# Performance work log

Hardware: AMD Instinct MI355X
Metric: run time of the kernel (lower is better)

## Reference

```python
import jax, jax.numpy as jnp
import numpy as np

TAU = 1.0
ATOL = 1e-06
MAX_ITER = 64  # bisection halves the bracket each iter; 64 iters reaches fp32 precision
N_WORKERS = 64
D = 2097152  # 2**21 coordinates


def setup_inputs() -> dict:
    key = jax.random.key(0)
    y = jax.random.normal(key, (N_WORKERS, D), dtype=jnp.float32)
    return {"y": y}


def reference(y) -> jnp.ndarray:
    # Coordinate-wise smooth (erf-based) median via bisection.
    # torch code transposes y and reduces over the last dim; equivalently we
    # reduce over the worker axis (axis 0) and keep per-coordinate state [d].
    xl = jnp.min(y, axis=0)  # [d] lower bracket
    xg = jnp.max(y, axis=0)  # [d] upper bracket

    def body(_, carry):
        xl, xg = carry
        xm = 0.5 * (xl + xg)                                  # [d]
        fm = jnp.sum(jax.lax.erf((y - xm) / TAU), axis=0)     # [d]
        left = fm > 0
        xl = jnp.where(left, xm, xl)
        xg = jnp.where(left, xg, xm)
        return xl, xg

    # Fixed trip count (no host-sync early exit). After MAX_ITER=64 halvings the
    # bracket width is far below the torch atol=1e-6 break threshold, so the
    # result matches the torch early-exit version to well within atol.
    xl, xg = jax.lax.fori_loop(0, MAX_ITER, body, (xl, xg))
    return 0.5 * (xl + xg)  # [d]
```

## Files before the change

### kernel.cpp

```cpp
#include <hip/hip_runtime.h>

typedef float v2f __attribute__((ext_vector_type(2)));

#define NW 64
#define NP 32
#define MAX_EVALS 8
#define FREEZE_TOL 7e-3f

__global__ __launch_bounds__(256, 4) void damed_median_kernel(
    const float* __restrict__ y, float* __restrict__ out, int D) {
  int d = blockIdx.x * blockDim.x + threadIdx.x;
  if (d >= D) return;

  v2f v[NP];
  v2f vmin = {3.4e38f, 3.4e38f}, vmax = {-3.4e38f, -3.4e38f}, sum2 = {0.f, 0.f};
#pragma unroll
  for (int p = 0; p < NP; ++p) {
    v2f t;
    t.x = y[(size_t)(2 * p) * (size_t)D + (size_t)d];
    t.y = y[(size_t)(2 * p + 1) * (size_t)D + (size_t)d];
    v[p] = t;
    vmin = __builtin_elementwise_min(vmin, t);
    vmax = __builtin_elementwise_max(vmax, t);
    sum2 += t;
  }
  float xl = fminf(vmin.x, vmin.y);
  float xg = fmaxf(vmax.x, vmax.y);
  float x = (sum2.x + sum2.y) * (1.0f / NW);
  x = fminf(fmaxf(x, xl), xg);

  const float B1 = 0.278393f, B2 = 0.230389f, B3 = 0.000972f, B4 = 0.078108f;
  const v2f one2 = {1.f, 1.f};
  const v2f Q1 = {B1, B1}, Q2 = {B2, B2}, Q3 = {B3, B3}, Q4 = {B4, B4};
  const v2f P1 = {B1, B1}, P2 = {2 * B2, 2 * B2};
  const v2f P3 = {3 * B3, 3 * B3}, P4 = {4 * B4, 4 * B4};

  auto evalF = [&](float xc) -> float {
    v2f fmA = {0.f, 0.f}, fmB = {0.f, 0.f};
    v2f nx = {-xc, -xc};
#pragma unroll
    for (int p = 0; p < NP; p += 2) {
      v2f tA = v[p] + nx;
      v2f tB = v[p + 1] + nx;
      v2f aA = __builtin_elementwise_max(tA, -tA);
      v2f aB = __builtin_elementwise_max(tB, -tB);
      v2f qA = __builtin_elementwise_fma(aA, Q4, Q3);
      v2f qB = __builtin_elementwise_fma(aB, Q4, Q3);
      qA = __builtin_elementwise_fma(aA, qA, Q2);
      qB = __builtin_elementwise_fma(aB, qB, Q2);
      qA = __builtin_elementwise_fma(aA, qA, Q1);
      qB = __builtin_elementwise_fma(aB, qB, Q1);
      qA = __builtin_elementwise_fma(aA, qA, one2);
      qB = __builtin_elementwise_fma(aB, qB, one2);
      v2f rA, rB;
      rA.x = __builtin_amdgcn_rcpf(qA.x); rA.y = __builtin_amdgcn_rcpf(qA.y);
      rB.x = __builtin_amdgcn_rcpf(qB.x); rB.y = __builtin_amdgcn_rcpf(qB.y);
      rA = rA * rA; rB = rB * rB;
      rA = rA * rA; rB = rB * rB;
      v2f eA = one2 - rA;
      v2f eB = one2 - rB;
      eA.x = __builtin_copysignf(eA.x, tA.x); eA.y = __builtin_copysignf(eA.y, tA.y);
      eB.x = __builtin_copysignf(eB.x, tB.x); eB.y = __builtin_copysignf(eB.y, tB.y);
      fmA += eA; fmB += eB;
    }
    v2f s = fmA + fmB;
    return s.x + s.y;
  };

  float fm0, fd0;
  {
    v2f fmA = {0.f, 0.f}, fmB = {0.f, 0.f}, fdA = {0.f, 0.f}, fdB = {0.f, 0.f};
    v2f nx = {-x, -x};
#pragma unroll
    for (int p = 0; p < NP; p += 2) {
      v2f tA = v[p] + nx;
      v2f tB = v[p + 1] + nx;
      v2f aA = __builtin_elementwise_max(tA, -tA);
      v2f aB = __builtin_elementwise_max(tB, -tB);
      v2f qA = __builtin_elementwise_fma(aA, Q4, Q3);
      v2f qB = __builtin_elementwise_fma(aB, Q4, Q3);
      qA = __builtin_elementwise_fma(aA, qA, Q2);
      qB = __builtin_elementwise_fma(aB, qB, Q2);
      qA = __builtin_elementwise_fma(aA, qA, Q1);
      qB = __builtin_elementwise_fma(aB, qB, Q1);
      qA = __builtin_elementwise_fma(aA, qA, one2);
      qB = __builtin_elementwise_fma(aB, qB, one2);
      v2f dA = __builtin_elementwise_fma(aA, P4, P3);
      v2f dB = __builtin_elementwise_fma(aB, P4, P3);
      dA = __builtin_elementwise_fma(aA, dA, P2);
      dB = __builtin_elementwise_fma(aB, dB, P2);
      dA = __builtin_elementwise_fma(aA, dA, P1);
      dB = __builtin_elementwise_fma(aB, dB, P1);
      v2f rA, rB;
      rA.x = __builtin_amdgcn_rcpf(qA.x); rA.y = __builtin_amdgcn_rcpf(qA.y);
      rB.x = __builtin_amdgcn_rcpf(qB.x); rB.y = __builtin_amdgcn_rcpf(qB.y);
      v2f r2A = rA * rA, r2B = rB * rB;
      v2f r4A = r2A * r2A, r4B = r2B * r2B;
      v2f r5A = r4A * rA, r5B = r4B * rB;
      fdA = __builtin_elementwise_fma(r5A, dA, fdA);
      fdB = __builtin_elementwise_fma(r5B, dB, fdB);
      v2f eA = one2 - r4A;
      v2f eB = one2 - r4B;
      eA.x = __builtin_copysignf(eA.x, tA.x); eA.y = __builtin_copysignf(eA.y, tA.y);
      eB.x = __builtin_copysignf(eB.x, tB.x); eB.y = __builtin_copysignf(eB.y, tB.y);
      fmA += eA; fmB += eB;
    }
    v2f fm2 = fmA + fmB, fd2 = fdA + fdB;
    fm0 = fm2.x + fm2.y;
    fd0 = 4.0f * (fd2.x + fd2.y);
  }
  if (fm0 > 0.f) xl = x; else xg = x;
  float xn = x + fm0 * __builtin_amdgcn_rcpf(fd0);
  bool ok = (xn >= xl) && (xn <= xg);
  float cand = ok ? xn : 0.5f * (xl + xg);
  bool frozen = (__builtin_fabsf(cand - x) <= FREEZE_TOL);
  float xprev = x, fmprev = fm0;
  x = cand;

#pragma unroll 1
  for (int e = 1; e < MAX_EVALS; ++e) {
    if (__all(frozen)) break;
    float fmc = evalF(x);
    if (fmc > 0.f) xl = x; else xg = x;
    float xs = x + fmc * (x - xprev) / (fmprev - fmc);
    bool ok2 = (xs >= xl) && (xs <= xg);
    float cand2 = ok2 ? xs : 0.5f * (xl + xg);
    float st = __builtin_fabsf(cand2 - x);
    bool done = (st <= FREEZE_TOL) || (fmc == 0.f);
    float xnew = frozen ? x : cand2;
    xprev = frozen ? xprev : x;
    fmprev = frozen ? fmprev : fmc;
    frozen = frozen || done;
    x = xnew;
  }
  out[d] = x;
}

extern "C" void kernel_launch(void* const* d_in, const int* in_sizes, int n_in,
                              void* d_out, int out_size, void* d_ws, size_t ws_size,
                              hipStream_t stream) {
  const float* y = (const float*)d_in[0];
  float* out = (float*)d_out;
  const int D = out_size;
  const int threads = 256;
  const int blocks = (D + threads - 1) / threads;
  damed_median_kernel<<<blocks, threads, 0, stream>>>(y, out, D);
}
```

Before: 117.4 us.

## Split each coordinate's workers across two lanes with shuffle reductions

Each coordinate is now handled by two lanes in the same wavefront, each holding 32 of the 64 worker values. Partial min, max, sum, f and f' values are combined with __shfl_xor across lane offset 32. This halves per-thread register storage so occupancy can rise (launch bounds go from 4 to 6), and doubles the thread count. The cost is extra shuffles per evaluation, and each 64-lane wave now covers only 32 coordinates, so both halves keep running until the whole wave has converged.

Result: slower. 126.0 us (+7.3%).

```diff
diff --git a/kernel.cpp b/kernel.cpp
--- a/kernel.cpp
+++ b/kernel.cpp
@@ -3,30 +3,37 @@
 typedef float v2f __attribute__((ext_vector_type(2)));
 
 #define NW 64
-#define NP 32
+#define NPL 16
 #define MAX_EVALS 8
 #define FREEZE_TOL 7e-3f
 
-__global__ __launch_bounds__(256, 4) void damed_median_kernel(
+__global__ __launch_bounds__(256, 6) void damed_median_kernel(
     const float* __restrict__ y, float* __restrict__ out, int D) {
-  int d = blockIdx.x * blockDim.x + threadIdx.x;
-  if (d >= D) return;
+  const int t = blockIdx.x * blockDim.x + threadIdx.x;
+  const int sub = (t >> 5) & 1;
+  const int dcoord = (t >> 6) * 32 + (t & 31);
+  const int dc = dcoord < D ? dcoord : D - 1;
+  const int wbase = sub * 32;
 
-  v2f v[NP];
+  v2f v[NPL];
   v2f vmin = {3.4e38f, 3.4e38f}, vmax = {-3.4e38f, -3.4e38f}, sum2 = {0.f, 0.f};
 #pragma unroll
-  for (int p = 0; p < NP; ++p) {
-    v2f t;
-    t.x = y[(size_t)(2 * p) * (size_t)D + (size_t)d];
-    t.y = y[(size_t)(2 * p + 1) * (size_t)D + (size_t)d];
-    v[p] = t;
-    vmin = __builtin_elementwise_min(vmin, t);
-    vmax = __builtin_elementwise_max(vmax, t);
-    sum2 += t;
+  for (int p = 0; p < NPL; ++p) {
+    v2f w;
+    w.x = y[(size_t)(wbase + 2 * p) * (size_t)D + (size_t)dc];
+    w.y = y[(size_t)(wbase + 2 * p + 1) * (size_t)D + (size_t)dc];
+    v[p] = w;
+    vmin = __builtin_elementwise_min(vmin, w);
+    vmax = __builtin_elementwise_max(vmax, w);
+    sum2 += w;
   }
   float xl = fminf(vmin.x, vmin.y);
   float xg = fmaxf(vmax.x, vmax.y);
-  float x = (sum2.x + sum2.y) * (1.0f / NW);
+  float sm = sum2.x + sum2.y;
+  xl = fminf(xl, __shfl_xor(xl, 32));
+  xg = fmaxf(xg, __shfl_xor(xg, 32));
+  sm = sm + __shfl_xor(sm, 32);
+  float x = sm * (1.0f / NW);
   x = fminf(fmaxf(x, xl), xg);
 
   const float B1 = 0.278393f, B2 = 0.230389f, B3 = 0.000972f, B4 = 0.078108f;
@@ -35,11 +42,11 @@
   const v2f P1 = {B1, B1}, P2 = {2 * B2, 2 * B2};
   const v2f P3 = {3 * B3, 3 * B3}, P4 = {4 * B4, 4 * B4};
 
-  auto evalF = [&](float xc) -> float {
+  auto evalHalf = [&](float xc) -> float {
     v2f fmA = {0.f, 0.f}, fmB = {0.f, 0.f};
     v2f nx = {-xc, -xc};
 #pragma unroll
-    for (int p = 0; p < NP; p += 2) {
+    for (int p = 0; p < NPL; p += 2) {
       v2f tA = v[p] + nx;
       v2f tB = v[p + 1] + nx;
       v2f aA = __builtin_elementwise_max(tA, -tA);
@@ -72,7 +79,7 @@
     v2f fmA = {0.f, 0.f}, fmB = {0.f, 0.f}, fdA = {0.f, 0.f}, fdB = {0.f, 0.f};
     v2f nx = {-x, -x};
 #pragma unroll
-    for (int p = 0; p < NP; p += 2) {
+    for (int p = 0; p < NPL; p += 2) {
       v2f tA = v[p] + nx;
       v2f tB = v[p + 1] + nx;
       v2f aA = __builtin_elementwise_max(tA, -tA);
@@ -106,8 +113,10 @@
       fmA += eA; fmB += eB;
     }
     v2f fm2 = fmA + fmB, fd2 = fdA + fdB;
-    fm0 = fm2.x + fm2.y;
-    fd0 = 4.0f * (fd2.x + fd2.y);
+    float fmh = fm2.x + fm2.y;
+    float fdh = fd2.x + fd2.y;
+    fm0 = fmh + __shfl_xor(fmh, 32);
+    fd0 = 4.0f * (fdh + __shfl_xor(fdh, 32));
   }
   if (fm0 > 0.f) xl = x; else xg = x;
   float xn = x + fm0 * __builtin_amdgcn_rcpf(fd0);
@@ -120,7 +129,8 @@
 #pragma unroll 1
   for (int e = 1; e < MAX_EVALS; ++e) {
     if (__all(frozen)) break;
-    float fmc = evalF(x);
+    float fmh = evalHalf(x);
+    float fmc = fmh + __shfl_xor(fmh, 32);
     if (fmc > 0.f) xl = x; else xg = x;
     float xs = x + fmc * (x - xprev) / (fmprev - fmc);
     bool ok2 = (xs >= xl) && (xs <= xg);
@@ -133,7 +143,7 @@
     frozen = frozen || done;
     x = xnew;
   }
-  out[d] = x;
+  if (sub == 0 && dcoord < D) out[dcoord] = x;
 }
 
 extern "C" void kernel_launch(void* const* d_in, const int* in_sizes, int n_in,
@@ -143,6 +153,6 @@
   float* out = (float*)d_out;
   const int D = out_size;
   const int threads = 256;
-  const int blocks = (D + threads - 1) / threads;
+  const int blocks = (D + 127) / 128;
   damed_median_kernel<<<blocks, threads, 0, stream>>>(y, out, D);
 }
```
